# Kernel optimization log

Hardware: AMD Instinct MI355X
Metric: run time of the kernel (lower is better)

Reference implementation:

```python
import jax, jax.numpy as jnp
import numpy as np

N = 100000
E = 3200000
F_IN = 512
HID = 16
C = 40


def setup_inputs() -> dict:
    key = jax.random.key(0)
    ks = jax.random.split(key, 6)
    x = jax.random.normal(ks[0], (N, F_IN), dtype=jnp.float32)
    edge_index = jax.random.randint(ks[1], (2, E), 0, N, dtype=jnp.int64)
    edge_weight = jax.random.uniform(ks[2], (E,), dtype=jnp.float32)
    # Glorot-style init like PyG GCNConv
    W1 = jax.random.normal(ks[3], (F_IN, HID), dtype=jnp.float32) * (1.0 / np.sqrt(F_IN))
    b1 = jnp.zeros((HID,), dtype=jnp.float32)
    W2 = jax.random.normal(ks[4], (HID, C), dtype=jnp.float32) * (1.0 / np.sqrt(HID))
    b2 = jnp.zeros((C,), dtype=jnp.float32)
    return {"x": x, "edge_index": edge_index, "edge_weight": edge_weight,
            "W1": W1, "b1": b1, "W2": W2, "b2": b2}


def _gcn_conv(h, W, b, row, col, norm, num_nodes):
    # h: [N, Fin] -> [N, Fout];  out = D^-1/2 A D^-1/2 (h W) + b, no self loops
    h = h @ W                                           # [N, Fout]
    msg = norm[:, None] * h[row]                        # gather + scale, [E, Fout]
    agg = jax.ops.segment_sum(msg, col, num_segments=num_nodes)  # scatter-add
    return agg + b


def reference(x, edge_index, edge_weight, W1, b1, W2, b2):
    num_nodes = x.shape[0]
    row, col = edge_index[0], edge_index[1]
    # symmetric gcn normalization (add_self_loops=False)
    deg = jax.ops.segment_sum(edge_weight, col, num_segments=num_nodes)  # [N]
    deg_inv_sqrt = jnp.where(deg > 0, jax.lax.rsqrt(jnp.maximum(deg, 1e-30)), 0.0)
    norm = deg_inv_sqrt[row] * edge_weight * deg_inv_sqrt[col]           # [E]

    h = jax.nn.relu(_gcn_conv(x, W1, b1, row, col, norm, num_nodes))
    # dropout is identity in eval mode (training=False)
    h = _gcn_conv(h, W2, b2, row, col, norm, num_nodes)
    return jax.nn.log_softmax(h, axis=-1)
```

## Files before the change

### kernel.cpp

```cpp
#include <hip/hip_runtime.h>

typedef float floatx4_t __attribute__((ext_vector_type(4)));
typedef __bf16 bf16x8_t __attribute__((ext_vector_type(8)));
typedef short shortx8_t __attribute__((ext_vector_type(8)));
typedef unsigned long long ull;

__device__ __forceinline__ unsigned short f2bf_rne(float f) {
    unsigned u = __float_as_uint(f);
    unsigned r = u + 0x7FFFu + ((u >> 16) & 1u);
    return (unsigned short)(r >> 16);
}
__device__ __forceinline__ float bf2f(unsigned short h) {
    return __uint_as_float((unsigned)h << 16);
}

#define MAXB 2048
#define CHUNK 8192
#define CAP 3072

__global__ __launch_bounds__(256) void k_scatter_gemm(const int* __restrict__ row,
                                                      const int* __restrict__ col,
                                                      const float* __restrict__ ew,
                                                      int* __restrict__ gcnt,
                                                      ull* __restrict__ packed,
                                                      const float* __restrict__ x,
                                                      const float* __restrict__ W1,
                                                      unsigned short* __restrict__ h1s,
                                                      int E, int B, int gC, int N) {
    int t = threadIdx.x;
    if ((int)blockIdx.x < gC) {
        __shared__ int h[MAXB];
        __shared__ int base[MAXB];
        for (int i = t; i < B; i += 256) h[i] = 0;
        __syncthreads();
        int cbase = blockIdx.x * CHUNK;
#pragma unroll 2
        for (int k = 0; k < 8; ++k) {
            int e = cbase + k * 1024 + t * 4;
            if (e + 3 < E) {
                int4 c4 = *(const int4*)(col + e);
                atomicAdd(&h[c4.x >> 6], 1);
                atomicAdd(&h[c4.y >> 6], 1);
                atomicAdd(&h[c4.z >> 6], 1);
                atomicAdd(&h[c4.w >> 6], 1);
            } else {
                for (int j = 0; j < 4; ++j)
                    if (e + j < E) atomicAdd(&h[col[e + j] >> 6], 1);
            }
        }
        __syncthreads();
        for (int i = t; i < B; i += 256) {
            int c = h[i];
            base[i] = c ? atomicAdd(&gcnt[i], c) : 0;
        }
        __syncthreads();
#pragma unroll 2
        for (int k = 0; k < 8; ++k) {
            int e = cbase + k * 1024 + t * 4;
            if (e + 3 < E) {
                int4 c4 = *(const int4*)(col + e);
                int4 r4 = *(const int4*)(row + e);
                float4 w4 = *(const float4*)(ew + e);
                int cs[4] = {c4.x, c4.y, c4.z, c4.w};
                int rs[4] = {r4.x, r4.y, r4.z, r4.w};
                float wsv[4] = {w4.x, w4.y, w4.z, w4.w};
#pragma unroll
                for (int j = 0; j < 4; ++j) {
                    int c = cs[j];
                    int b = c >> 6;
                    int pos = atomicAdd(&base[b], 1);
                    if (pos < CAP) {
                        ull hi = (ull)(unsigned)((rs[j] << 6) | (c & 63)) << 32;
                        packed[(size_t)b * CAP + pos] = hi | (unsigned)__float_as_uint(wsv[j]);
                    }
                }
            } else {
                for (int j = 0; j < 4; ++j) {
                    if (e + j < E) {
                        int c = col[e + j];
                        int b = c >> 6;
                        int pos = atomicAdd(&base[b], 1);
                        if (pos < CAP) {
                            ull hi = (ull)(unsigned)((row[e + j] << 6) | (c & 63)) << 32;
                            packed[(size_t)b * CAP + pos] = hi | (unsigned)__float_as_uint(ew[e + j]);
                        }
                    }
                }
            }
        }
    } else {
        int b = blockIdx.x - gC;
        const int lane = t & 63;
        const int wave = t >> 6;
        const int m = lane & 15;
        const int q = lane >> 4;
        const int nbase = b * 64 + wave * 16;

        shortx8_t bs[16];
#pragma unroll
        for (int c = 0; c < 16; ++c) {
#pragma unroll
            for (int j = 0; j < 8; ++j) {
                int k = c * 32 + q * 8 + j;
                bs[c][j] = (short)f2bf_rne(W1[k * 16 + m]);
            }
        }

        int rowi = nbase + m;
        if (rowi >= N) rowi = N - 1;
        const float* xr = x + (size_t)rowi * 512;

        floatx4_t acc = {0.f, 0.f, 0.f, 0.f};
#pragma unroll
        for (int c = 0; c < 16; ++c) {
            const float4 u0 = *(const float4*)(xr + c * 32 + q * 8);
            const float4 u1 = *(const float4*)(xr + c * 32 + q * 8 + 4);
            shortx8_t as;
            as[0] = (short)f2bf_rne(u0.x); as[1] = (short)f2bf_rne(u0.y);
            as[2] = (short)f2bf_rne(u0.z); as[3] = (short)f2bf_rne(u0.w);
            as[4] = (short)f2bf_rne(u1.x); as[5] = (short)f2bf_rne(u1.y);
            as[6] = (short)f2bf_rne(u1.z); as[7] = (short)f2bf_rne(u1.w);
            acc = __builtin_amdgcn_mfma_f32_16x16x32_bf16(
                __builtin_bit_cast(bf16x8_t, as),
                __builtin_bit_cast(bf16x8_t, bs[c]), acc, 0, 0, 0);
        }

#pragma unroll
        for (int r = 0; r < 4; ++r) {
            int node = nbase + q * 4 + r;
            if (node < N)
                h1s[(size_t)node * 16 + m] = f2bf_rne(acc[r]);
        }
    }
}

__global__ __launch_bounds__(256) void k_sortdis(const int* __restrict__ gcnt,
                                                 const ull* __restrict__ packed,
                                                 unsigned* __restrict__ packed2,
                                                 int2* __restrict__ rng,
                                                 float* __restrict__ dis, int N) {
    __shared__ int cnt[64];
    __shared__ int cur[64];
    __shared__ float dacc[64];
    int t = threadIdx.x;
    if (t < 64) { cnt[t] = 0; dacc[t] = 0.f; }
    __syncthreads();
    int b = blockIdx.x;
    size_t gbase = (size_t)b * CAP;
    int szr = gcnt[b];
    int sz = szr < CAP ? szr : CAP;

    for (int j = t; j < sz; j += 256) {
        ull p = packed[gbase + j];
        int nd = (int)(p >> 32) & 63;
        atomicAdd(&cnt[nd], 1);
        atomicAdd(&dacc[nd], __uint_as_float((unsigned)p));
    }
    __syncthreads();
    if (t < 64) {
        int c = cnt[t];
        int xp = c;
#pragma unroll
        for (int off = 1; off < 64; off <<= 1) {
            int y = __shfl_up(xp, off);
            if (t >= off) xp += y;
        }
        int off0 = xp - c;
        cur[t] = off0;
        float s = dacc[t];
        float d = (s > 0.f) ? rsqrtf(s) : 0.f;
        int g = b * 64 + t;
        if (g < N) {
            rng[g] = make_int2((int)gbase + off0, (int)gbase + off0 + c);
            dis[g] = d;
        }
    }
    __syncthreads();
    for (int j = t; j < sz; j += 256) {
        ull p = packed[gbase + j];
        int nd = (int)(p >> 32) & 63;
        int r = (int)(p >> 32) >> 6;
        unsigned short wb = f2bf_rne(__uint_as_float((unsigned)p));
        int pos = atomicAdd(&cur[nd], 1);
        packed2[gbase + pos] = ((unsigned)r << 15) | (unsigned)wb;
    }
}

__global__ __launch_bounds__(256) void k_agg1(const int2* __restrict__ rng,
                                              const unsigned* __restrict__ packed2,
                                              const float* __restrict__ dis,
                                              const unsigned short* __restrict__ h1s,
                                              const float* __restrict__ b1,
                                              unsigned short* __restrict__ hs, int N) {
    int wv = (blockIdx.x * 256 + threadIdx.x) >> 6;
    if (wv >= N) return;
    int lane = threadIdx.x & 63;
    int e4 = lane >> 4, f = lane & 15;
    int2 r2 = rng[wv];
    int beg = r2.x, end = r2.y;
    float a0 = 0.f, a1 = 0.f, a2 = 0.f, a3 = 0.f;
    int i = beg + e4;
    for (; i + 12 < end; i += 16) {
        unsigned p0 = packed2[i];
        unsigned p1 = packed2[i + 4];
        unsigned p2 = packed2[i + 8];
        unsigned p3 = packed2[i + 12];
        int r0 = p0 >> 15, r1 = p1 >> 15, r2i = p2 >> 15, r3 = p3 >> 15;
        a0 += __uint_as_float((p0 & 0x7FFFu) << 16) * dis[r0] * bf2f(h1s[(size_t)r0 * 16 + f]);
        a1 += __uint_as_float((p1 & 0x7FFFu) << 16) * dis[r1] * bf2f(h1s[(size_t)r1 * 16 + f]);
        a2 += __uint_as_float((p2 & 0x7FFFu) << 16) * dis[r2i] * bf2f(h1s[(size_t)r2i * 16 + f]);
        a3 += __uint_as_float((p3 & 0x7FFFu) << 16) * dis[r3] * bf2f(h1s[(size_t)r3 * 16 + f]);
    }
    for (; i < end; i += 4) {
        unsigned p = packed2[i];
        int r = p >> 15;
        a0 += __uint_as_float((p & 0x7FFFu) << 16) * dis[r] * bf2f(h1s[(size_t)r * 16 + f]);
    }
    float a = (a0 + a1) + (a2 + a3);
    a += __shfl_xor(a, 16);
    a += __shfl_xor(a, 32);
    if (e4 == 0) {
        float dg = dis[wv];
        float v = dg * a + b1[f];
        v = (v > 0.f) ? v : 0.f;
        hs[(size_t)wv * 16 + f] = f2bf_rne(v);
    }
}

__global__ __launch_bounds__(256) void k_agg2out(const int2* __restrict__ rng,
                                                 const unsigned* __restrict__ packed2,
                                                 const float* __restrict__ dis,
                                                 const unsigned short* __restrict__ hs,
                                                 const float* __restrict__ W2,
                                                 const float* __restrict__ b2,
                                                 float* __restrict__ out, int N) {
    int wv = (blockIdx.x * 256 + threadIdx.x) >> 6;
    if (wv >= N) return;
    int lane = threadIdx.x & 63;
    int e4 = lane >> 4, f = lane & 15;
    int2 r2 = rng[wv];
    int beg = r2.x, end = r2.y;
    float a0 = 0.f, a1 = 0.f, a2 = 0.f, a3 = 0.f;
    int i = beg + e4;
    for (; i + 12 < end; i += 16) {
        unsigned p0 = packed2[i];
        unsigned p1 = packed2[i + 4];
        unsigned p2 = packed2[i + 8];
        unsigned p3 = packed2[i + 12];
        int r0 = p0 >> 15, r1 = p1 >> 15, r2i = p2 >> 15, r3 = p3 >> 15;
        a0 += __uint_as_float((p0 & 0x7FFFu) << 16) * dis[r0] * bf2f(hs[(size_t)r0 * 16 + f]);
        a1 += __uint_as_float((p1 & 0x7FFFu) << 16) * dis[r1] * bf2f(hs[(size_t)r1 * 16 + f]);
        a2 += __uint_as_float((p2 & 0x7FFFu) << 16) * dis[r2i] * bf2f(hs[(size_t)r2i * 16 + f]);
        a3 += __uint_as_float((p3 & 0x7FFFu) << 16) * dis[r3] * bf2f(hs[(size_t)r3 * 16 + f]);
    }
    for (; i < end; i += 4) {
        unsigned p = packed2[i];
        int r = p >> 15;
        a0 += __uint_as_float((p & 0x7FFFu) << 16) * dis[r] * bf2f(hs[(size_t)r * 16 + f]);
    }
    float a = (a0 + a1) + (a2 + a3);
    a += __shfl_xor(a, 16);
    a += __shfl_xor(a, 32);

    float dg = dis[wv];
    int c = lane;
    int cc = (c < 40) ? c : 39;
    float z = 0.f;
#pragma unroll
    for (int fi = 0; fi < 16; ++fi) {
        float af = __shfl(a, fi);
        z += af * W2[fi * 40 + cc];
    }
    z = dg * z + b2[cc];

    float zm = (c < 40) ? z : -3.4e38f;
#pragma unroll
    for (int off = 1; off < 64; off <<= 1) zm = fmaxf(zm, __shfl_xor(zm, off));
    float ex = (c < 40) ? __expf(z - zm) : 0.f;
    float s = ex;
#pragma unroll
    for (int off = 1; off < 64; off <<= 1) s += __shfl_xor(s, off);
    float lse = zm + __logf(s);
    if (c < 40) out[(size_t)wv * 40 + c] = z - lse;
}

extern "C" void kernel_launch(void* const* d_in, const int* in_sizes, int n_in,
                              void* d_out, int out_size, void* d_ws, size_t ws_size,
                              hipStream_t stream) {
    const float* x  = (const float*)d_in[0];
    const int*   ei = (const int*)d_in[1];
    const float* ew = (const float*)d_in[2];
    const float* W1 = (const float*)d_in[3];
    const float* b1 = (const float*)d_in[4];
    const float* W2 = (const float*)d_in[5];
    const float* b2 = (const float*)d_in[6];

    const int N = in_sizes[0] / 512;
    const int E = in_sizes[2];
    const int* row = ei;
    const int* col = ei + E;
    const int B = (N + 63) >> 6;

    ull*      packed  = (ull*)d_ws;
    unsigned* packed2 = (unsigned*)(packed + (size_t)B * CAP);
    int*      gcnt    = (int*)(packed2 + (size_t)B * CAP);
    int2*     rng     = (int2*)(gcnt + B + (B & 1));
    float*    dis     = (float*)(rng + N);
    unsigned short* h1s = (unsigned short*)(dis + N);
    unsigned short* hs  = h1s + (size_t)16 * N;

    hipMemsetAsync(gcnt, 0, (size_t)B * sizeof(int), stream);

    const int gC = (E + CHUNK - 1) / CHUNK;
    const int gW = (N * 64 + 255) / 256;

    k_scatter_gemm<<<gC + B, 256, 0, stream>>>(row, col, ew, gcnt, packed,
                                               x, W1, h1s, E, B, gC, N);
    k_sortdis<<<B, 256, 0, stream>>>(gcnt, packed, packed2, rng, dis, N);
    k_agg1<<<gW, 256, 0, stream>>>(rng, packed2, dis, h1s, b1, hs, N);
    k_agg2out<<<gW, 256, 0, stream>>>(rng, packed2, dis, hs, W2, b2, (float*)d_out, N);
}
```

Measured before the change: 512.7 us.

## Prescale features by source degree norm and compute degrees via global atomics

Per-node edge counts and weighted degrees are now accumulated with global atomics in the scatter kernel, which removes the first pass over packed edges in the sort kernel. The sort kernel then prescales the layer-1 features by each source's inverse-sqrt degree. Layer-1 features are stored as fp32 rather than bf16, and layer 2's input is prescaled the same way, so both aggregation loops drop the per-edge dis[r] gather. The cost is 6.4M extra global atomics, a doubled h1 gather footprint, and a larger memset.

```diff
diff --git a/kernel.cpp b/kernel.cpp
--- a/kernel.cpp
+++ b/kernel.cpp
@@ -22,10 +22,12 @@
                                                       const int* __restrict__ col,
                                                       const float* __restrict__ ew,
                                                       int* __restrict__ gcnt,
+                                                      int* __restrict__ ncnt,
+                                                      float* __restrict__ degw,
                                                       ull* __restrict__ packed,
                                                       const float* __restrict__ x,
                                                       const float* __restrict__ W1,
-                                                      unsigned short* __restrict__ h1s,
+                                                      float* __restrict__ h1f,
                                                       int E, int B, int gC, int N) {
     int t = threadIdx.x;
     if ((int)blockIdx.x < gC) {
@@ -68,6 +70,8 @@
                 for (int j = 0; j < 4; ++j) {
                     int c = cs[j];
                     int b = c >> 6;
+                    atomicAdd(&ncnt[c], 1);
+                    atomicAdd(&degw[c], wsv[j]);
                     int pos = atomicAdd(&base[b], 1);
                     if (pos < CAP) {
                         ull hi = (ull)(unsigned)((rs[j] << 6) | (c & 63)) << 32;
@@ -79,6 +83,8 @@
                     if (e + j < E) {
                         int c = col[e + j];
                         int b = c >> 6;
+                        atomicAdd(&ncnt[c], 1);
+                        atomicAdd(&degw[c], ew[e + j]);
                         int pos = atomicAdd(&base[b], 1);
                         if (pos < CAP) {
                             ull hi = (ull)(unsigned)((row[e + j] << 6) | (c & 63)) << 32;
@@ -129,36 +135,30 @@
         for (int r = 0; r < 4; ++r) {
             int node = nbase + q * 4 + r;
             if (node < N)
-                h1s[(size_t)node * 16 + m] = f2bf_rne(acc[r]);
+                h1f[(size_t)node * 16 + m] = acc[r];
         }
     }
 }
 
 __global__ __launch_bounds__(256) void k_sortdis(const int* __restrict__ gcnt,
+                                                 const int* __restrict__ ncnt,
+                                                 const float* __restrict__ degw,
                                                  const ull* __restrict__ packed,
                                                  unsigned* __restrict__ packed2,
                                                  int2* __restrict__ rng,
-                                                 float* __restrict__ dis, int N) {
-    __shared__ int cnt[64];
+                                                 float* __restrict__ dis,
+                                                 float* __restrict__ h1f, int N) {
     __shared__ int cur[64];
-    __shared__ float dacc[64];
+    __shared__ float sdis[64];
     int t = threadIdx.x;
-    if (t < 64) { cnt[t] = 0; dacc[t] = 0.f; }
-    __syncthreads();
     int b = blockIdx.x;
     size_t gbase = (size_t)b * CAP;
     int szr = gcnt[b];
     int sz = szr < CAP ? szr : CAP;
 
-    for (int j = t; j < sz; j += 256) {
-        ull p = packed[gbase + j];
-        int nd = (int)(p >> 32) & 63;
-        atomicAdd(&cnt[nd], 1);
-        atomicAdd(&dacc[nd], __uint_as_float((unsigned)p));
-    }
-    __syncthreads();
     if (t < 64) {
-        int c = cnt[t];
+        int g = b * 64 + t;
+        int c = (g < N) ? ncnt[g] : 0;
         int xp = c;
 #pragma unroll
         for (int off = 1; off < 64; off <<= 1) {
@@ -166,30 +166,44 @@
             if (t >= off) xp += y;
         }
         int off0 = xp - c;
-        cur[t] = off0;
-        float s = dacc[t];
+        if (off0 > CAP) off0 = CAP;
+        int e = off0 + c;
+        if (e > CAP) e = CAP;
+        cur[t] = (int)gbase + off0;
+        float s = (g < N) ? degw[g] : 0.f;
         float d = (s > 0.f) ? rsqrtf(s) : 0.f;
-        int g = b * 64 + t;
+        sdis[t] = d;
         if (g < N) {
-            rng[g] = make_int2((int)gbase + off0, (int)gbase + off0 + c);
+            rng[g] = make_int2((int)gbase + off0, (int)gbase + e);
             dis[g] = d;
         }
     }
     __syncthreads();
+    int capend = (int)gbase + CAP;
     for (int j = t; j < sz; j += 256) {
         ull p = packed[gbase + j];
-        int nd = (int)(p >> 32) & 63;
-        int r = (int)(p >> 32) >> 6;
+        int hi = (int)(p >> 32);
+        int nd = hi & 63;
+        int r = hi >> 6;
         unsigned short wb = f2bf_rne(__uint_as_float((unsigned)p));
         int pos = atomicAdd(&cur[nd], 1);
-        packed2[gbase + pos] = ((unsigned)r << 15) | (unsigned)wb;
+        if (pos < capend)
+            packed2[pos] = ((unsigned)r << 15) | (unsigned)wb;
+    }
+    for (int k = t; k < 1024; k += 256) {
+        int n = k >> 4, f = k & 15;
+        int node = b * 64 + n;
+        if (node < N) {
+            size_t idx = (size_t)node * 16 + f;
+            h1f[idx] = sdis[n] * h1f[idx];
+        }
     }
 }
 
 __global__ __launch_bounds__(256) void k_agg1(const int2* __restrict__ rng,
                                               const unsigned* __restrict__ packed2,
                                               const float* __restrict__ dis,
-                                              const unsigned short* __restrict__ h1s,
+                                              const float* __restrict__ h1f,
                                               const float* __restrict__ b1,
                                               unsigned short* __restrict__ hs, int N) {
     int wv = (blockIdx.x * 256 + threadIdx.x) >> 6;
@@ -206,15 +220,15 @@
         unsigned p2 = packed2[i + 8];
         unsigned p3 = packed2[i + 12];
         int r0 = p0 >> 15, r1 = p1 >> 15, r2i = p2 >> 15, r3 = p3 >> 15;
-        a0 += __uint_as_float((p0 & 0x7FFFu) << 16) * dis[r0] * bf2f(h1s[(size_t)r0 * 16 + f]);
-        a1 += __uint_as_float((p1 & 0x7FFFu) << 16) * dis[r1] * bf2f(h1s[(size_t)r1 * 16 + f]);
-        a2 += __uint_as_float((p2 & 0x7FFFu) << 16) * dis[r2i] * bf2f(h1s[(size_t)r2i * 16 + f]);
-        a3 += __uint_as_float((p3 & 0x7FFFu) << 16) * dis[r3] * bf2f(h1s[(size_t)r3 * 16 + f]);
+        a0 += __uint_as_float((p0 & 0x7FFFu) << 16) * h1f[(size_t)r0 * 16 + f];
+        a1 += __uint_as_float((p1 & 0x7FFFu) << 16) * h1f[(size_t)r1 * 16 + f];
+        a2 += __uint_as_float((p2 & 0x7FFFu) << 16) * h1f[(size_t)r2i * 16 + f];
+        a3 += __uint_as_float((p3 & 0x7FFFu) << 16) * h1f[(size_t)r3 * 16 + f];
     }
     for (; i < end; i += 4) {
         unsigned p = packed2[i];
         int r = p >> 15;
-        a0 += __uint_as_float((p & 0x7FFFu) << 16) * dis[r] * bf2f(h1s[(size_t)r * 16 + f]);
+        a0 += __uint_as_float((p & 0x7FFFu) << 16) * h1f[(size_t)r * 16 + f];
     }
     float a = (a0 + a1) + (a2 + a3);
     a += __shfl_xor(a, 16);
@@ -223,7 +237,7 @@
         float dg = dis[wv];
         float v = dg * a + b1[f];
         v = (v > 0.f) ? v : 0.f;
-        hs[(size_t)wv * 16 + f] = f2bf_rne(v);
+        hs[(size_t)wv * 16 + f] = f2bf_rne(dg * v);
     }
 }
 
@@ -248,15 +262,15 @@
         unsigned p2 = packed2[i + 8];
         unsigned p3 = packed2[i + 12];
         int r0 = p0 >> 15, r1 = p1 >> 15, r2i = p2 >> 15, r3 = p3 >> 15;
-        a0 += __uint_as_float((p0 & 0x7FFFu) << 16) * dis[r0] * bf2f(hs[(size_t)r0 * 16 + f]);
-        a1 += __uint_as_float((p1 & 0x7FFFu) << 16) * dis[r1] * bf2f(hs[(size_t)r1 * 16 + f]);
-        a2 += __uint_as_float((p2 & 0x7FFFu) << 16) * dis[r2i] * bf2f(hs[(size_t)r2i * 16 + f]);
-        a3 += __uint_as_float((p3 & 0x7FFFu) << 16) * dis[r3] * bf2f(hs[(size_t)r3 * 16 + f]);
+        a0 += __uint_as_float((p0 & 0x7FFFu) << 16) * bf2f(hs[(size_t)r0 * 16 + f]);
+        a1 += __uint_as_float((p1 & 0x7FFFu) << 16) * bf2f(hs[(size_t)r1 * 16 + f]);
+        a2 += __uint_as_float((p2 & 0x7FFFu) << 16) * bf2f(hs[(size_t)r2i * 16 + f]);
+        a3 += __uint_as_float((p3 & 0x7FFFu) << 16) * bf2f(hs[(size_t)r3 * 16 + f]);
     }
     for (; i < end; i += 4) {
         unsigned p = packed2[i];
         int r = p >> 15;
-        a0 += __uint_as_float((p & 0x7FFFu) << 16) * dis[r] * bf2f(hs[(size_t)r * 16 + f]);
+        a0 += __uint_as_float((p & 0x7FFFu) << 16) * bf2f(hs[(size_t)r * 16 + f]);
     }
     float a = (a0 + a1) + (a2 + a3);
     a += __shfl_xor(a, 16);
@@ -300,23 +314,26 @@
     const int* row = ei;
     const int* col = ei + E;
     const int B = (N + 63) >> 6;
+    const int Npad = B * 64;
 
     ull*      packed  = (ull*)d_ws;
     unsigned* packed2 = (unsigned*)(packed + (size_t)B * CAP);
     int*      gcnt    = (int*)(packed2 + (size_t)B * CAP);
-    int2*     rng     = (int2*)(gcnt + B + (B & 1));
+    int*      ncnt    = gcnt + B + 1;
+    float*    degw    = (float*)(ncnt + Npad);
+    int2*     rng     = (int2*)(degw + Npad);
     float*    dis     = (float*)(rng + N);
-    unsigned short* h1s = (unsigned short*)(dis + N);
-    unsigned short* hs  = h1s + (size_t)16 * N;
-
-    hipMemsetAsync(gcnt, 0, (size_t)B * sizeof(int), stream);
+    float*    h1f     = dis + N;
+    unsigned short* hs = (unsigned short*)(h1f + (size_t)16 * Npad);
+
+    hipMemsetAsync(gcnt, 0, ((size_t)B + 1 + 2 * (size_t)Npad) * sizeof(int), stream);
 
     const int gC = (E + CHUNK - 1) / CHUNK;
     const int gW = (N * 64 + 255) / 256;
 
-    k_scatter_gemm<<<gC + B, 256, 0, stream>>>(row, col, ew, gcnt, packed,
-                                               x, W1, h1s, E, B, gC, N);
-    k_sortdis<<<B, 256, 0, stream>>>(gcnt, packed, packed2, rng, dis, N);
-    k_agg1<<<gW, 256, 0, stream>>>(rng, packed2, dis, h1s, b1, hs, N);
+    k_scatter_gemm<<<gC + B, 256, 0, stream>>>(row, col, ew, gcnt, ncnt, degw, packed,
+                                               x, W1, h1f, E, B, gC, N);
+    k_sortdis<<<B, 256, 0, stream>>>(gcnt, ncnt, degw, packed, packed2, rng, dis, h1f, N);
+    k_agg1<<<gW, 256, 0, stream>>>(rng, packed2, dis, h1f, b1, hs, N);
     k_agg2out<<<gW, 256, 0, stream>>>(rng, packed2, dis, hs, W2, b2, (float*)d_out, N);
 }
```

Measured after the change: 703.7 us. +37.3%, slower.
